# Optimization experiments

Hardware: AMD Instinct MI355X
Metric: run time of the kernel (lower is better)

## Reference

```python
import jax, jax.numpy as jnp
import numpy as np

B, S, H = 2, 2048, 1024
NH, DH = 16, 64  # num heads, head dim

def setup_inputs() -> dict:
    key = jax.random.key(0)
    ks = jax.random.split(key, 4)
    scale = 0.02
    return {
        "hidden_states": jax.random.normal(ks[0], (B, S, H), dtype=jnp.float32),
        "attention_mask": jnp.zeros((B, 1, 1, S), dtype=jnp.float32),  # additive mask
        "Wq": jax.random.normal(ks[1], (H, H), dtype=jnp.float32) * scale,
        "bq": jnp.zeros((H,), dtype=jnp.float32),
        "Wk": jax.random.normal(ks[2], (H, H), dtype=jnp.float32) * scale,
        "bk": jnp.zeros((H,), dtype=jnp.float32),
        "Wv": jax.random.normal(ks[3], (H, H), dtype=jnp.float32) * scale,
        "bv": jnp.zeros((H,), dtype=jnp.float32),
    }

def _split_heads(x):
    # [B,S,H] -> [B,NH,S,DH]
    return x.reshape(B, S, NH, DH).transpose(0, 2, 1, 3)

def reference(hidden_states, attention_mask, Wq, bq, Wk, bk, Wv, bv):
    q = _split_heads(hidden_states @ Wq + bq)
    k = _split_heads(hidden_states @ Wk + bk)
    v = _split_heads(hidden_states @ Wv + bv)
    # scores: [B,NH,S,S]
    scores = jnp.einsum('bhqd,bhkd->bhqk', q, k) / jnp.asarray(np.sqrt(DH), scores_dtype := q.dtype)
    scores = scores + attention_mask  # additive mask broadcast
    probs = jax.nn.softmax(scores, axis=-1)
    out = jnp.einsum('bhqk,bhkd->bhqd', probs, v)  # [B,NH,S,DH]
    out = out.transpose(0, 2, 1, 3).reshape(B, S, H)
    return out
```

## Files before the change

### kernel.cpp

```cpp
#include <hip/hip_runtime.h>
#include <hip/hip_bf16.h>

#define Bn  2
#define Sn  2048
#define Hn  1024
#define NHn 16
#define DHn 64
#define Mn  (Bn * Sn)

typedef __attribute__((ext_vector_type(4)))  float    f32x4;
typedef __attribute__((ext_vector_type(16))) float    f32x16;
typedef __attribute__((ext_vector_type(8)))  _Float16 h8;
typedef __attribute__((ext_vector_type(4)))  _Float16 h4;
typedef __attribute__((ext_vector_type(2)))  unsigned int u32x2;

union H2U  { _Float16 h[2]; unsigned int u; };
union U4H8 { unsigned int u[4]; h8 v; };

#define MFMA16F(a, b, c) __builtin_amdgcn_mfma_f32_16x16x32_f16(a, b, c, 0, 0, 0)
#define MFMA32F(a, b, c) __builtin_amdgcn_mfma_f32_32x32x16_f16(a, b, c, 0, 0, 0)

__device__ __forceinline__ void glds16(const void* g, void* l) {
    __builtin_amdgcn_global_load_lds(
        (const __attribute__((address_space(1))) unsigned int*)g,
        (__attribute__((address_space(3))) unsigned int*)l, 16, 0, 0);
}

__global__ __launch_bounds__(256) void cvt_x(
    const float* __restrict__ X, _Float16* __restrict__ Xh)
{
    const int i = blockIdx.x * 256 + threadIdx.x;
    float4 x = ((const float4*)X)[i];
    h4 o;
    o[0] = (_Float16)x.x; o[1] = (_Float16)x.y;
    o[2] = (_Float16)x.z; o[3] = (_Float16)x.w;
    *(h4*)&Xh[(size_t)i * 4] = o;
}

__global__ __launch_bounds__(256) void cvt_wT(
    const float* __restrict__ W0, const float* __restrict__ W1,
    const float* __restrict__ W2, _Float16* __restrict__ WT)
{
    const int which = blockIdx.z;
    const float* W = (which == 0) ? W0 : (which == 1 ? W1 : W2);
    _Float16* O = WT + (size_t)which * Hn * Hn;

    const int k0 = blockIdx.x * 64;
    const int n0 = blockIdx.y * 64;
    const int tid = threadIdx.x;

    __shared__ float Ws[64][65];

#pragma unroll
    for (int it = 0; it < 4; ++it) {
        const int idx = tid + 256 * it;
        const int row = idx >> 4, c4 = (idx & 15) * 4;
        float4 w = *(const float4*)&W[(size_t)(k0 + row) * Hn + n0 + c4];
        Ws[row][c4 + 0] = w.x; Ws[row][c4 + 1] = w.y;
        Ws[row][c4 + 2] = w.z; Ws[row][c4 + 3] = w.w;
    }
    __syncthreads();
#pragma unroll
    for (int it = 0; it < 16; ++it) {
        const int e = tid + 256 * it;
        const int k = e & 63, n = e >> 6;
        O[(size_t)(n0 + n) * Hn + k0 + k] = (_Float16)Ws[k][n];
    }
}

__global__ __launch_bounds__(256) void qkv_mfma(
    const _Float16* __restrict__ Xh, const _Float16* __restrict__ WTA,
    const float* __restrict__ b0, const float* __restrict__ b1,
    const float* __restrict__ b2,
    _Float16* __restrict__ Qh, _Float16* __restrict__ Kh,
    _Float16* __restrict__ VTh)
{
    const int which = blockIdx.z;
    const _Float16* WT = WTA + (size_t)which * Hn * Hn;
    const float* bias = (which == 0) ? b0 : (which == 1 ? b1 : b2);
    _Float16* Dst = (which == 0) ? Qh : (which == 1 ? Kh : VTh);

    const int m0 = blockIdx.x * 128;
    const int n0 = blockIdx.y * 128;
    const int tid  = threadIdx.x;
    const int wid  = tid >> 6;
    const int lane = tid & 63;
    const int l16  = lane & 15;
    const int quad = lane >> 4;
    const int wm = wid >> 1, wn = wid & 1;

    __shared__ _Float16 Ah[128 * 32], Bh[128 * 32];

    f32x4 acc[4][4];
#pragma unroll
    for (int i = 0; i < 4; ++i)
#pragma unroll
        for (int j = 0; j < 4; ++j) acc[i][j] = (f32x4){0.f, 0.f, 0.f, 0.f};

    for (int kt = 0; kt < Hn / 32; ++kt) {
        const int k0 = kt * 32;
        __syncthreads();
#pragma unroll
        for (int c = 0; c < 2; ++c) {
            const int idx = (wid * 2 + c) * 64 + lane;
            const int row = idx >> 2;
            const int cg  = (idx & 3) ^ (row & 3);
            glds16(&Xh[(size_t)(m0 + row) * Hn + k0 + cg * 8],
                   &Ah[(wid * 2 + c) * 512]);
            glds16(&WT[(size_t)(n0 + row) * Hn + k0 + cg * 8],
                   &Bh[(wid * 2 + c) * 512]);
        }
        __syncthreads();

        h8 xa[4], wb[4];
#pragma unroll
        for (int t = 0; t < 4; ++t) {
            const int ar = wm * 64 + t * 16 + l16;
            const int br = wn * 64 + t * 16 + l16;
            xa[t] = *(const h8*)&Ah[ar * 32 + ((quad ^ (ar & 3)) * 8)];
            wb[t] = *(const h8*)&Bh[br * 32 + ((quad ^ (br & 3)) * 8)];
        }
        if (which < 2) {
#pragma unroll
            for (int i = 0; i < 4; ++i)
#pragma unroll
                for (int j = 0; j < 4; ++j)
                    acc[i][j] = MFMA16F(xa[i], wb[j], acc[i][j]);
        } else {
#pragma unroll
            for (int i = 0; i < 4; ++i)
#pragma unroll
                for (int j = 0; j < 4; ++j)
                    acc[i][j] = MFMA16F(wb[i], xa[j], acc[i][j]);
        }
    }

    if (which < 2) {
#pragma unroll
        for (int j = 0; j < 4; ++j) {
            const int n = n0 + wn * 64 + j * 16 + l16;
            const float bv = bias[n];
            const int hh = n >> 6, dd = n & 63;
#pragma unroll
            for (int i = 0; i < 4; ++i) {
                const int mb = m0 + wm * 64 + i * 16 + quad * 4;
#pragma unroll
                for (int r = 0; r < 4; ++r) {
                    const int m = mb + r;
                    const int b = m >> 11, s = m & (Sn - 1);
                    Dst[(((size_t)b * NHn + hh) * Sn + s) * DHn + dd] =
                        (_Float16)(acc[i][j][r] + bv);
                }
            }
        }
    } else {
#pragma unroll
        for (int i = 0; i < 4; ++i) {
#pragma unroll
            for (int r = 0; r < 4; ++r) {
                const int n = n0 + wn * 64 + i * 16 + quad * 4 + r;
                const float bv = bias[n];
                const int hh = n >> 6, dd = n & 63;
#pragma unroll
                for (int j = 0; j < 4; ++j) {
                    const int m = m0 + wm * 64 + j * 16 + l16;
                    const int b = m >> 11, s = m & (Sn - 1);
                    Dst[(((size_t)b * NHn + hh) * DHn + dd) * Sn + s] =
                        (_Float16)(acc[i][j][r] + bv);
                }
            }
        }
    }
}

__global__ __launch_bounds__(256) void attn(
    const _Float16* __restrict__ Qh, const _Float16* __restrict__ Kh,
    const _Float16* __restrict__ VTh, const float* __restrict__ mask,
    float* __restrict__ Out)
{
    const int flat = blockIdx.x + 16 * blockIdx.y + 256 * blockIdx.z;
    const int bh   = ((flat & 7) << 2) | ((flat >> 3) & 3);
    const int qb   = flat >> 5;
    const int b = bh >> 4, h = bh & 15;

    const int tid  = threadIdx.x;
    const int wid  = tid >> 6;
    const int lane = tid & 63;
    const int l32  = lane & 31;
    const int hi   = lane >> 5;

    __shared__ __align__(16) _Float16 Kb[3][4096];
    __shared__ __align__(16) _Float16 Vb[3][4096];
    __shared__ float4 Ml4[Sn / 4];
    __shared__ float  Ilds[4][32];
    const float* Ml = (const float*)Ml4;

    const int q0 = qb * 128 + wid * 32;

    const size_t qbase = ((size_t)bh * Sn + q0 + l32) * DHn;
    h8 qf[4];
#pragma unroll
    for (int kd = 0; kd < 4; ++kd)
        qf[kd] = *(const h8*)&Qh[qbase + kd * 16 + hi * 8];

    {
        const float4* mg = (const float4*)(mask + (size_t)b * Sn);
        float4 m0 = mg[tid], m1 = mg[tid + 256];
        const float L2E = 1.44269504088896340736f;
        float4 a0 = {m0.x * L2E, m0.y * L2E, m0.z * L2E, m0.w * L2E};
        float4 a1 = {m1.x * L2E, m1.y * L2E, m1.z * L2E, m1.w * L2E};
        Ml4[tid] = a0;
        Ml4[tid + 256] = a1;
    }

    const _Float16* Kg = Kh  + (size_t)bh * Sn * DHn;
    const _Float16* Vg = VTh + (size_t)bh * DHn * Sn;

    auto stage = [&](int kt, int buf) {
        const int koff = kt * 64;
#pragma unroll
        for (int c = 0; c < 2; ++c) {
            const int idx = (wid * 2 + c) * 64 + lane;
            const int row = idx >> 3;
            const int cg  = (idx & 7) ^ (row & 7);
            glds16(&Kg[(size_t)(koff + row) * DHn + cg * 8],
                   &Kb[buf][(wid * 2 + c) * 512]);
            glds16(&Vg[(size_t)row * Sn + koff + cg * 8],
                   &Vb[buf][(wid * 2 + c) * 512]);
        }
    };

    stage(0, 0);
    stage(1, 1);
    asm volatile("s_waitcnt lgkmcnt(0)" ::: "memory");

    f32x16 o[2];
#pragma unroll
    for (int dt = 0; dt < 2; ++dt) o[dt] = (f32x16)(0.f);
    float l_lane = 0.f;

    int cur = 0;
    for (int kt = 0; kt < Sn / 64; ++kt) {
        if (kt < Sn / 64 - 1) asm volatile("s_waitcnt vmcnt(4)" ::: "memory");
        else                  asm volatile("s_waitcnt vmcnt(0)" ::: "memory");
        __builtin_amdgcn_s_barrier();
        asm volatile("" ::: "memory");

        if (kt + 2 < Sn / 64) {
            int stb = cur - 1; if (stb < 0) stb = 2;
            stage(kt + 2, stb);
        }

        f32x16 s[2];
        __builtin_amdgcn_s_setprio(1);
#pragma unroll
        for (int t = 0; t < 2; ++t) {
            f32x16 c = (f32x16)(0.f);
#pragma unroll
            for (int kd = 0; kd < 4; ++kd) {
                const int row = t * 32 + l32;
                h8 kf = *(const h8*)&Kb[cur][row * 64 +
                                             (((kd * 2 + hi) ^ (row & 7)) * 8)];
                c = MFMA32F(kf, qf[kd], c);
            }
            s[t] = c;
        }
        __builtin_amdgcn_s_setprio(0);

        const float SC = 0.18033688011112042f;
        unsigned int pk[2][4][2];
#pragma unroll
        for (int t = 0; t < 2; ++t) {
#pragma unroll
            for (int g = 0; g < 4; ++g) {
                float4 mv = *(const float4*)&Ml[kt * 64 + t * 32 + hi * 4 + g * 8];
                const float p0 = __builtin_amdgcn_exp2f(s[t][g * 4 + 0] * SC + mv.x);
                const float p1 = __builtin_amdgcn_exp2f(s[t][g * 4 + 1] * SC + mv.y);
                const float p2 = __builtin_amdgcn_exp2f(s[t][g * 4 + 2] * SC + mv.z);
                const float p3 = __builtin_amdgcn_exp2f(s[t][g * 4 + 3] * SC + mv.w);
                l_lane += (p0 + p1) + (p2 + p3);
                H2U a, c2;
                a.h[0]  = (_Float16)p0; a.h[1]  = (_Float16)p1;
                c2.h[0] = (_Float16)p2; c2.h[1] = (_Float16)p3;
                pk[t][g][0] = a.u; pk[t][g][1] = c2.u;
            }
        }

        __builtin_amdgcn_s_setprio(1);
#pragma unroll
        for (int ks = 0; ks < 4; ++ks) {
            const int t = ks >> 1, ge = (ks & 1) * 2;
            u32x2 rA = __builtin_amdgcn_permlane32_swap(
                pk[t][ge][0], pk[t][ge + 1][0], false, false);
            u32x2 rB = __builtin_amdgcn_permlane32_swap(
                pk[t][ge][1], pk[t][ge + 1][1], false, false);
            U4H8 w;
            w.u[0] = rA[0]; w.u[1] = rB[0]; w.u[2] = rA[1]; w.u[3] = rB[1];
#pragma unroll
            for (int dt = 0; dt < 2; ++dt) {
                const int row = dt * 32 + l32;
                h8 vf = *(const h8*)&Vb[cur][row * 64 +
                                             (((ks * 2 + hi) ^ (row & 7)) * 8)];
                o[dt] = MFMA32F(w.v, vf, o[dt]);
            }
        }
        __builtin_amdgcn_s_setprio(0);

        cur = (cur == 2) ? 0 : cur + 1;
    }

    const float l_tot = l_lane + __shfl_xor(l_lane, 32);
    if (lane < 32) Ilds[wid][l32] = 1.0f / l_tot;

#pragma unroll
    for (int g2 = 0; g2 < 4; ++g2) {
        float4 iv = *(const float4*)&Ilds[wid][hi * 4 + g2 * 8];
#pragma unroll
        for (int e = 0; e < 4; ++e) {
            const int r = g2 * 4 + e;
            const int q = q0 + 4 * hi + 8 * g2 + e;
            const size_t ob = ((size_t)b * Sn + q) * Hn + h * DHn;
            const float sc = ((const float*)&iv)[e];
#pragma unroll
            for (int dt = 0; dt < 2; ++dt)
                Out[ob + dt * 32 + l32] = o[dt][r] * sc;
        }
    }
}

extern "C" void kernel_launch(void* const* d_in, const int* in_sizes, int n_in,
                              void* d_out, int out_size, void* d_ws, size_t ws_size,
                              hipStream_t stream) {
    const float* X    = (const float*)d_in[0];
    const float* mask = (const float*)d_in[1];
    const float* Wq   = (const float*)d_in[2];
    const float* bq   = (const float*)d_in[3];
    const float* Wk   = (const float*)d_in[4];
    const float* bk   = (const float*)d_in[5];
    const float* Wv   = (const float*)d_in[6];
    const float* bv   = (const float*)d_in[7];
    float* out = (float*)d_out;

    const size_t NE = (size_t)Mn * Hn;
    _Float16* Xh  = (_Float16*)d_ws;
    _Float16* WT  = Xh + NE;
    _Float16* Qh  = WT + (size_t)3 * Hn * Hn;
    _Float16* Kh  = Qh + NE;
    _Float16* VTh = Kh + NE;

    cvt_x<<<dim3(Mn * Hn / 1024), dim3(256), 0, stream>>>(X, Xh);
    cvt_wT<<<dim3(16, 16, 3), dim3(256), 0, stream>>>(Wq, Wk, Wv, WT);

    dim3 g1(Mn / 128, Hn / 128, 3), b1(256);
    qkv_mfma<<<g1, b1, 0, stream>>>(Xh, WT, bq, bk, bv, Qh, Kh, VTh);

    dim3 g2(Sn / 128, NHn, Bn), b2(256);
    attn<<<g2, b2, 0, stream>>>(Qh, Kh, VTh, mask, out);
}
```

Baseline: 184.2 us.

## Software-pipeline QK^T with softmax-PV, compute row sums via MFMA, merge prep kernels

Restructures the attention loop so the QK^T MFMAs for the next tile are issued before the softmax and PV work of the current tile. This uses two score register sets and a 4-deep K/V LDS ring with one barrier per iteration. Row sums of probabilities are accumulated by an extra MFMA against a ones vector instead of scalar adds plus a shuffle/LDS reduction, and packing uses cvt_pkrtz. It also merges the two conversion kernels into one launch and adds a launch_bounds occupancy hint of 2 blocks. It costs more registers and LDS (64KB K/V), and the row sums use the fp16-rounded probabilities.

```diff
diff --git a/kernel.cpp b/kernel.cpp
--- a/kernel.cpp
+++ b/kernel.cpp
@@ -12,9 +12,10 @@
 typedef __attribute__((ext_vector_type(16))) float    f32x16;
 typedef __attribute__((ext_vector_type(8)))  _Float16 h8;
 typedef __attribute__((ext_vector_type(4)))  _Float16 h4;
+typedef __attribute__((ext_vector_type(2)))  __fp16   fp16x2;
 typedef __attribute__((ext_vector_type(2)))  unsigned int u32x2;
 
-union H2U  { _Float16 h[2]; unsigned int u; };
+union H2PK { fp16x2 v; unsigned int u; };
 union U4H8 { unsigned int u[4]; h8 v; };
 
 #define MFMA16F(a, b, c) __builtin_amdgcn_mfma_f32_16x16x32_f16(a, b, c, 0, 0, 0)
@@ -26,30 +27,32 @@
         (__attribute__((address_space(3))) unsigned int*)l, 16, 0, 0);
 }
 
-__global__ __launch_bounds__(256) void cvt_x(
-    const float* __restrict__ X, _Float16* __restrict__ Xh)
+__global__ __launch_bounds__(256) void prep(
+    const float* __restrict__ X, const float* __restrict__ W0,
+    const float* __restrict__ W1, const float* __restrict__ W2,
+    _Float16* __restrict__ Xh, _Float16* __restrict__ WT)
 {
-    const int i = blockIdx.x * 256 + threadIdx.x;
-    float4 x = ((const float4*)X)[i];
-    h4 o;
-    o[0] = (_Float16)x.x; o[1] = (_Float16)x.y;
-    o[2] = (_Float16)x.z; o[3] = (_Float16)x.w;
-    *(h4*)&Xh[(size_t)i * 4] = o;
-}
-
-__global__ __launch_bounds__(256) void cvt_wT(
-    const float* __restrict__ W0, const float* __restrict__ W1,
-    const float* __restrict__ W2, _Float16* __restrict__ WT)
-{
-    const int which = blockIdx.z;
+    const int bid = blockIdx.x;
+    const int tid = threadIdx.x;
+    __shared__ float Ws[64][65];
+
+    if (bid < 4096) {
+        const int i = bid * 256 + tid;
+        float4 x = ((const float4*)X)[i];
+        h4 o;
+        o[0] = (_Float16)x.x; o[1] = (_Float16)x.y;
+        o[2] = (_Float16)x.z; o[3] = (_Float16)x.w;
+        *(h4*)&Xh[(size_t)i * 4] = o;
+        return;
+    }
+
+    const int wb = bid - 4096;
+    const int which = wb >> 8;
+    const int rem = wb & 255;
+    const int k0 = ((rem >> 4) & 15) * 64;
+    const int n0 = (rem & 15) * 64;
     const float* W = (which == 0) ? W0 : (which == 1 ? W1 : W2);
     _Float16* O = WT + (size_t)which * Hn * Hn;
-
-    const int k0 = blockIdx.x * 64;
-    const int n0 = blockIdx.y * 64;
-    const int tid = threadIdx.x;
-
-    __shared__ float Ws[64][65];
 
 #pragma unroll
     for (int it = 0; it < 4; ++it) {
@@ -173,7 +176,7 @@
     }
 }
 
-__global__ __launch_bounds__(256) void attn(
+__global__ __launch_bounds__(256, 2) void attn(
     const _Float16* __restrict__ Qh, const _Float16* __restrict__ Kh,
     const _Float16* __restrict__ VTh, const float* __restrict__ mask,
     float* __restrict__ Out)
@@ -189,13 +192,15 @@
     const int l32  = lane & 31;
     const int hi   = lane >> 5;
 
-    __shared__ __align__(16) _Float16 Kb[3][4096];
-    __shared__ __align__(16) _Float16 Vb[3][4096];
+    __shared__ __align__(16) _Float16 Kb[4][4096];
+    __shared__ __align__(16) _Float16 Vb[4][4096];
     __shared__ float4 Ml4[Sn / 4];
-    __shared__ float  Ilds[4][32];
     const float* Ml = (const float*)Ml4;
 
     const int q0 = qb * 128 + wid * 32;
+
+    const float4* mg = (const float4*)(mask + (size_t)b * Sn);
+    float4 m0v = mg[tid], m1v = mg[tid + 256];
 
     const size_t qbase = ((size_t)bh * Sn + q0 + l32) * DHn;
     h8 qf[4];
@@ -203,12 +208,12 @@
     for (int kd = 0; kd < 4; ++kd)
         qf[kd] = *(const h8*)&Qh[qbase + kd * 16 + hi * 8];
 
+    asm volatile("s_waitcnt vmcnt(0)" ::: "memory");
+
     {
-        const float4* mg = (const float4*)(mask + (size_t)b * Sn);
-        float4 m0 = mg[tid], m1 = mg[tid + 256];
         const float L2E = 1.44269504088896340736f;
-        float4 a0 = {m0.x * L2E, m0.y * L2E, m0.z * L2E, m0.w * L2E};
-        float4 a1 = {m1.x * L2E, m1.y * L2E, m1.z * L2E, m1.w * L2E};
+        float4 a0 = {m0v.x * L2E, m0v.y * L2E, m0v.z * L2E, m0v.w * L2E};
+        float4 a1 = {m1v.x * L2E, m1v.y * L2E, m1v.z * L2E, m1v.w * L2E};
         Ml4[tid] = a0;
         Ml4[tid + 256] = a1;
     }
@@ -232,26 +237,17 @@
 
     stage(0, 0);
     stage(1, 1);
-    asm volatile("s_waitcnt lgkmcnt(0)" ::: "memory");
-
-    f32x16 o[2];
+
+    f32x16 sA[2], sB[2], o[2], acc_l;
 #pragma unroll
     for (int dt = 0; dt < 2; ++dt) o[dt] = (f32x16)(0.f);
-    float l_lane = 0.f;
-
-    int cur = 0;
-    for (int kt = 0; kt < Sn / 64; ++kt) {
-        if (kt < Sn / 64 - 1) asm volatile("s_waitcnt vmcnt(4)" ::: "memory");
-        else                  asm volatile("s_waitcnt vmcnt(0)" ::: "memory");
-        __builtin_amdgcn_s_barrier();
-        asm volatile("" ::: "memory");
-
-        if (kt + 2 < Sn / 64) {
-            int stb = cur - 1; if (stb < 0) stb = 2;
-            stage(kt + 2, stb);
-        }
-
-        f32x16 s[2];
+    acc_l = (f32x16)(0.f);
+
+    h8 ones;
+#pragma unroll
+    for (int j = 0; j < 8; ++j) ones[j] = (_Float16)1.0f;
+
+    auto qkt = [&](f32x16 (&s)[2], int buf) {
         __builtin_amdgcn_s_setprio(1);
 #pragma unroll
         for (int t = 0; t < 2; ++t) {
@@ -259,14 +255,16 @@
 #pragma unroll
             for (int kd = 0; kd < 4; ++kd) {
                 const int row = t * 32 + l32;
-                h8 kf = *(const h8*)&Kb[cur][row * 64 +
+                h8 kf = *(const h8*)&Kb[buf][row * 64 +
                                              (((kd * 2 + hi) ^ (row & 7)) * 8)];
                 c = MFMA32F(kf, qf[kd], c);
             }
             s[t] = c;
         }
         __builtin_amdgcn_s_setprio(0);
-
+    };
+
+    auto sm_pv = [&](f32x16 (&s)[2], int kt, int buf) {
         const float SC = 0.18033688011112042f;
         unsigned int pk[2][4][2];
 #pragma unroll
@@ -278,11 +276,11 @@
                 const float p1 = __builtin_amdgcn_exp2f(s[t][g * 4 + 1] * SC + mv.y);
                 const float p2 = __builtin_amdgcn_exp2f(s[t][g * 4 + 2] * SC + mv.z);
                 const float p3 = __builtin_amdgcn_exp2f(s[t][g * 4 + 3] * SC + mv.w);
-                l_lane += (p0 + p1) + (p2 + p3);
-                H2U a, c2;
-                a.h[0]  = (_Float16)p0; a.h[1]  = (_Float16)p1;
-                c2.h[0] = (_Float16)p2; c2.h[1] = (_Float16)p3;
-                pk[t][g][0] = a.u; pk[t][g][1] = c2.u;
+                H2PK u0, u1;
+                u0.v = __builtin_amdgcn_cvt_pkrtz(p0, p1);
+                u1.v = __builtin_amdgcn_cvt_pkrtz(p2, p3);
+                pk[t][g][0] = u0.u;
+                pk[t][g][1] = u1.u;
             }
         }
 
@@ -296,31 +294,48 @@
                 pk[t][ge][1], pk[t][ge + 1][1], false, false);
             U4H8 w;
             w.u[0] = rA[0]; w.u[1] = rB[0]; w.u[2] = rA[1]; w.u[3] = rB[1];
+            acc_l = MFMA32F(w.v, ones, acc_l);
 #pragma unroll
             for (int dt = 0; dt < 2; ++dt) {
                 const int row = dt * 32 + l32;
-                h8 vf = *(const h8*)&Vb[cur][row * 64 +
+                h8 vf = *(const h8*)&Vb[buf][row * 64 +
                                              (((ks * 2 + hi) ^ (row & 7)) * 8)];
                 o[dt] = MFMA32F(w.v, vf, o[dt]);
             }
         }
         __builtin_amdgcn_s_setprio(0);
-
-        cur = (cur == 2) ? 0 : cur + 1;
-    }
-
-    const float l_tot = l_lane + __shfl_xor(l_lane, 32);
-    if (lane < 32) Ilds[wid][l32] = 1.0f / l_tot;
+    };
+
+    asm volatile("s_waitcnt vmcnt(4) lgkmcnt(0)" ::: "memory");
+    __builtin_amdgcn_s_barrier();
+    qkt(sA, 0);
+
+    auto iter = [&](int kt, f32x16 (&scur)[2], f32x16 (&snxt)[2]) {
+        stage(kt + 2, (kt + 2) & 3);
+        asm volatile("s_waitcnt vmcnt(4)" ::: "memory");
+        __builtin_amdgcn_s_barrier();
+        qkt(snxt, (kt + 1) & 3);
+        sm_pv(scur, kt, kt & 3);
+    };
+
+    for (int kt = 0; kt < 30; kt += 2) {
+        iter(kt,     sA, sB);
+        iter(kt + 1, sB, sA);
+    }
+    asm volatile("s_waitcnt vmcnt(0)" ::: "memory");
+    __builtin_amdgcn_s_barrier();
+    qkt(sB, 31 & 3);
+    sm_pv(sA, 30, 30 & 3);
+    sm_pv(sB, 31, 31 & 3);
 
 #pragma unroll
     for (int g2 = 0; g2 < 4; ++g2) {
-        float4 iv = *(const float4*)&Ilds[wid][hi * 4 + g2 * 8];
 #pragma unroll
         for (int e = 0; e < 4; ++e) {
             const int r = g2 * 4 + e;
             const int q = q0 + 4 * hi + 8 * g2 + e;
             const size_t ob = ((size_t)b * Sn + q) * Hn + h * DHn;
-            const float sc = ((const float*)&iv)[e];
+            const float sc = 1.0f / acc_l[r];
 #pragma unroll
             for (int dt = 0; dt < 2; ++dt)
                 Out[ob + dt * 32 + l32] = o[dt][r] * sc;
@@ -348,8 +363,7 @@
     _Float16* Kh  = Qh + NE;
     _Float16* VTh = Kh + NE;
 
-    cvt_x<<<dim3(Mn * Hn / 1024), dim3(256), 0, stream>>>(X, Xh);
-    cvt_wT<<<dim3(16, 16, 3), dim3(256), 0, stream>>>(Wq, Wk, Wv, WT);
+    prep<<<dim3(4096 + 768), dim3(256), 0, stream>>>(X, Wq, Wk, Wv, Xh, WT);
 
     dim3 g1(Mn / 128, Hn / 128, 3), b1(256);
     qkv_mfma<<<g1, b1, 0, stream>>>(Xh, WT, bq, bk, bv, Qh, Kh, VTh);
```

Measured after the change: 177.2 us. 1.04x faster.
